# Kernel tuning notes

Hardware: AMD Instinct MI355X
Metric: run time of the kernel (lower is better)

Reference implementation:

```python
import jax, jax.numpy as jnp
import numpy as np

EPS = 0.001

def _conv1x1(h, w, b):
    # h: [n,c,v,w_dim], w: [o,c], b: [o]  -> [n,o,v,w_dim]
    return jnp.einsum('ncvw,oc->novw', h, w) + b[None, :, None, None]

def setup_inputs() -> dict:
    key = jax.random.key(0)
    ks = jax.random.split(key, 10)
    N, Cin, T, V = 16, 64, 64, 384
    inp = {
        'x': jax.random.normal(ks[0], (N, Cin, T, V), dtype=jnp.float32),
        'A': jax.random.uniform(ks[1], (N, 8, V, V), dtype=jnp.float32),
        'conv_w': jax.random.normal(ks[2], (64, Cin), dtype=jnp.float32) * 0.05,
        'conv_b': jax.random.normal(ks[3], (64,), dtype=jnp.float32) * 0.05,
        'w1': jax.random.normal(ks[4], (16, 7), dtype=jnp.float32) * 0.2,
        'b1': jax.random.normal(ks[5], (16,), dtype=jnp.float32) * 0.05,
        'w2': jax.random.normal(ks[6], (32, 16), dtype=jnp.float32) * 0.2,
        'b2': jax.random.normal(ks[7], (32,), dtype=jnp.float32) * 0.05,
        'w3': jax.random.normal(ks[8], (64, 32), dtype=jnp.float32) * 0.2,
        'b3': jax.random.normal(ks[9], (64,), dtype=jnp.float32) * 0.05,
    }
    return inp

def reference(x, A, conv_w, conv_b, w1, b1, w2, b2, w3, b3):
    # self.conv: 1x1 conv (t_kernel_size=1) mapping in_channels -> out_channels*kernel_size = 64
    x = jnp.einsum('nctv,oc->notv', x, conv_w) + conv_b[None, :, None, None]
    mask = A[:, 7][:, None]              # [n,1,v,w]
    h = A[:, :7]                         # [n,7,v,w]
    # adjmatder: three 1x1 convs with ReLU (dropout = identity in eval mode)
    h = jax.nn.relu(_conv1x1(h, w1, b1))
    h = jax.nn.relu(_conv1x1(h, w2, b2))
    h = jax.nn.relu(_conv1x1(h, w3, b3))   # [n,64,v,w]
    Am = h * mask
    Dl = 1.0 / (Am.sum(axis=2) + EPS)      # degree-inverse over v: [n,64,w]
    An = Am * Dl[:, :, None, :]            # einsum 'ncvw,ncw->ncvw'
    out = jnp.einsum('nctv,ncvw->nctw', x, An)
    return out, An
```

## Files before the change

### kernel.cpp

```cpp
#include <hip/hip_runtime.h>

#define EPS_F 0.001f

constexpr int Nn = 16;
constexpr int Cc = 64;
constexpr int Tt = 64;
constexpr int Vv = 384;
constexpr size_t TV = (size_t)Tt * Vv;
constexpr size_t VW = (size_t)Vv * Vv;
constexpr size_t OUT0 = (size_t)Nn * Cc * TV;

__global__ __launch_bounds__(256) void k_conv(const float* __restrict__ x,
        const float* __restrict__ cw, const float* __restrict__ cb,
        float* __restrict__ xc) {
    __shared__ float wt[64 * 64];
    const int tid = threadIdx.x;
    for (int i = tid; i < 4096; i += 256) {
        int o = i & 63, c = i >> 6;
        wt[c * 64 + o] = cw[o * 64 + c];
    }
    __syncthreads();
    const int b = blockIdx.x;
    const int n = b / 48;
    const int pos = (b % 48) * 512 + tid;
    const float* xin = x + (size_t)n * Cc * TV + pos;
    float acc0[64], acc1[64];
#pragma unroll
    for (int o = 0; o < 64; ++o) { acc0[o] = 0.f; acc1[o] = 0.f; }
    for (int c = 0; c < 64; ++c) {
        float x0 = xin[(size_t)c * TV];
        float x1 = xin[(size_t)c * TV + 256];
        const float4* wr = (const float4*)(wt + c * 64);
#pragma unroll
        for (int oq = 0; oq < 16; ++oq) {
            float4 w4 = wr[oq];
            acc0[oq*4+0] += x0 * w4.x; acc0[oq*4+1] += x0 * w4.y;
            acc0[oq*4+2] += x0 * w4.z; acc0[oq*4+3] += x0 * w4.w;
            acc1[oq*4+0] += x1 * w4.x; acc1[oq*4+1] += x1 * w4.y;
            acc1[oq*4+2] += x1 * w4.z; acc1[oq*4+3] += x1 * w4.w;
        }
    }
    float* xo = xc + (size_t)n * Cc * TV + pos;
#pragma unroll
    for (int o = 0; o < 64; ++o) {
        float bo = cb[o];
        xo[(size_t)o * TV]       = acc0[o] + bo;
        xo[(size_t)o * TV + 256] = acc1[o] + bo;
    }
}

__device__ __forceinline__ void mlp12(const float a[8],
        const float* __restrict__ w1, const float* __restrict__ b1,
        const float* __restrict__ w2, const float* __restrict__ b2,
        float h2[32]) {
    float h1[16];
#pragma unroll
    for (int o = 0; o < 16; ++o) {
        float t = b1[o];
#pragma unroll
        for (int k = 0; k < 7; ++k) t += w1[o * 7 + k] * a[k];
        h1[o] = fmaxf(t, 0.f);
    }
#pragma unroll
    for (int o = 0; o < 32; ++o) {
        float t = b2[o];
#pragma unroll
        for (int i = 0; i < 16; ++i) t += w2[o * 16 + i] * h1[i];
        h2[o] = fmaxf(t, 0.f);
    }
}

__global__ __launch_bounds__(384) void k_am(const float* __restrict__ A,
        const float* __restrict__ w1, const float* __restrict__ b1,
        const float* __restrict__ w2, const float* __restrict__ b2,
        const float* __restrict__ w3, const float* __restrict__ b3,
        float* __restrict__ Am) {
    const int tid = threadIdx.x;
    const int b = blockIdx.x;
    const int n = b / 384;
    const int v = b % 384;
    const float* Ab = A + (size_t)n * 8 * VW + (size_t)v * Vv + tid;
    float a[8];
#pragma unroll
    for (int k = 0; k < 8; ++k) a[k] = Ab[(size_t)k * VW];
    float h2[32];
    mlp12(a, w1, b1, w2, b2, h2);
    const float mask = a[7];
    float* ap = Am + (size_t)n * 64 * VW + (size_t)v * Vv + tid;
#pragma unroll
    for (int o = 0; o < 64; ++o) {
        float t = b3[o];
#pragma unroll
        for (int i = 0; i < 32; ++i) t += w3[o * 32 + i] * h2[i];
        ap[(size_t)o * VW] = fmaxf(t, 0.f) * mask;
    }
}

__global__ __launch_bounds__(384) void k_red(const float* __restrict__ Am,
        float* __restrict__ Dlr) {
    __shared__ float4 part[4][96];
    const int tid = threadIdx.x;
    const int wi = tid % 96;
    const int vq = tid / 96;
    const int b = blockIdx.x;
    const float4* p = (const float4*)(Am + (size_t)b * VW) + wi;
    float4 s = make_float4(0.f, 0.f, 0.f, 0.f);
#pragma unroll 4
    for (int v = vq * 96; v < vq * 96 + 96; ++v) {
        float4 t = p[(size_t)v * 96];
        s.x += t.x; s.y += t.y; s.z += t.z; s.w += t.w;
    }
    part[vq][wi] = s;
    __syncthreads();
    if (vq == 0) {
        float4 s0 = part[0][wi], s1 = part[1][wi], s2 = part[2][wi], s3 = part[3][wi];
        float4 r;
        r.x = 1.f / ((s0.x + s1.x) + (s2.x + s3.x) + EPS_F);
        r.y = 1.f / ((s0.y + s1.y) + (s2.y + s3.y) + EPS_F);
        r.z = 1.f / ((s0.z + s1.z) + (s2.z + s3.z) + EPS_F);
        r.w = 1.f / ((s0.w + s1.w) + (s2.w + s3.w) + EPS_F);
        *((float4*)(Dlr + (size_t)b * Vv) + wi) = r;
    }
}

__global__ __launch_bounds__(256) void k_gemm(const float* __restrict__ xc,
        float* __restrict__ An, const float* __restrict__ Dlr,
        float* __restrict__ out) {
    __shared__ float As[16 * 68];
    __shared__ float Bs[16 * 68];
    const int tid = threadIdx.x;
    const int b = blockIdx.x;
    const int batch = b / 6;
    const int w0 = (b % 6) * 64;
    const float* Ap = xc + (size_t)batch * TV;
    float* Bp = An + (size_t)batch * VW + w0;
    const int ty = tid / 16, tx = tid % 16;
    const int lr = tid / 4,  lq = tid % 4;
    const int br = tid / 16, bc = tid % 16;
    const float4 dl4 = *(const float4*)(Dlr + (size_t)batch * Vv + w0 + bc * 4);
    float acc[4][4];
#pragma unroll
    for (int i = 0; i < 4; ++i)
#pragma unroll
        for (int j = 0; j < 4; ++j) acc[i][j] = 0.f;
    for (int k0 = 0; k0 < 384; k0 += 16) {
        float4 a4 = *(const float4*)(Ap + (size_t)lr * 384 + k0 + lq * 4);
        float4 b4 = *(const float4*)(Bp + (size_t)(k0 + br) * 384 + bc * 4);
        b4.x *= dl4.x; b4.y *= dl4.y; b4.z *= dl4.z; b4.w *= dl4.w;
        *(float4*)(Bp + (size_t)(k0 + br) * 384 + bc * 4) = b4;
        As[(lq*4+0)*68 + lr] = a4.x;
        As[(lq*4+1)*68 + lr] = a4.y;
        As[(lq*4+2)*68 + lr] = a4.z;
        As[(lq*4+3)*68 + lr] = a4.w;
        *(float4*)(Bs + br * 68 + bc * 4) = b4;
        __syncthreads();
#pragma unroll
        for (int kk = 0; kk < 16; ++kk) {
            float4 av = *(const float4*)(As + kk * 68 + ty * 4);
            float4 bv = *(const float4*)(Bs + kk * 68 + tx * 4);
            float aa[4] = {av.x, av.y, av.z, av.w};
            float bb[4] = {bv.x, bv.y, bv.z, bv.w};
#pragma unroll
            for (int i = 0; i < 4; ++i)
#pragma unroll
                for (int j = 0; j < 4; ++j) acc[i][j] += aa[i] * bb[j];
        }
        __syncthreads();
    }
    float* op = out + (size_t)batch * TV + w0 + tx * 4;
#pragma unroll
    for (int i = 0; i < 4; ++i) {
        float4 o4 = make_float4(acc[i][0], acc[i][1], acc[i][2], acc[i][3]);
        *(float4*)(op + (size_t)(ty * 4 + i) * 384) = o4;
    }
}

extern "C" void kernel_launch(void* const* d_in, const int* in_sizes, int n_in,
                              void* d_out, int out_size, void* d_ws, size_t ws_size,
                              hipStream_t stream) {
    const float* x  = (const float*)d_in[0];
    const float* A  = (const float*)d_in[1];
    const float* cw = (const float*)d_in[2];
    const float* cb = (const float*)d_in[3];
    const float* w1 = (const float*)d_in[4];
    const float* b1 = (const float*)d_in[5];
    const float* w2 = (const float*)d_in[6];
    const float* b2 = (const float*)d_in[7];
    const float* w3 = (const float*)d_in[8];
    const float* b3 = (const float*)d_in[9];

    float* out = (float*)d_out;
    float* An  = out + OUT0;
    float* xc  = (float*)d_ws;
    float* Dlr = xc + OUT0;

    k_conv<<<768, 256, 0, stream>>>(x, cw, cb, xc);
    k_am  <<<6144, 384, 0, stream>>>(A, w1, b1, w2, b2, w3, b3, An);
    k_red <<<1024, 384, 0, stream>>>(An, Dlr);
    k_gemm<<<6144, 256, 0, stream>>>(xc, An, Dlr, out);
}
```

Baseline: 1.461 ms.

## Fuse degree reduction into GEMM and apply normalization after accumulation

Removes the separate column-sum kernel; the GEMM block accumulates column sums of Am while loading tiles, computes the inverse degree in shared memory, scales the output accumulators, then rescales An in place in a second pass. This drops one kernel launch and one global read of Am but adds a reread of the block's Am slice, which may be served from cache.

```diff
diff --git a/kernel.cpp b/kernel.cpp
--- a/kernel.cpp
+++ b/kernel.cpp
@@ -96,38 +96,12 @@
     }
 }
 
-__global__ __launch_bounds__(384) void k_red(const float* __restrict__ Am,
-        float* __restrict__ Dlr) {
-    __shared__ float4 part[4][96];
-    const int tid = threadIdx.x;
-    const int wi = tid % 96;
-    const int vq = tid / 96;
-    const int b = blockIdx.x;
-    const float4* p = (const float4*)(Am + (size_t)b * VW) + wi;
-    float4 s = make_float4(0.f, 0.f, 0.f, 0.f);
-#pragma unroll 4
-    for (int v = vq * 96; v < vq * 96 + 96; ++v) {
-        float4 t = p[(size_t)v * 96];
-        s.x += t.x; s.y += t.y; s.z += t.z; s.w += t.w;
-    }
-    part[vq][wi] = s;
-    __syncthreads();
-    if (vq == 0) {
-        float4 s0 = part[0][wi], s1 = part[1][wi], s2 = part[2][wi], s3 = part[3][wi];
-        float4 r;
-        r.x = 1.f / ((s0.x + s1.x) + (s2.x + s3.x) + EPS_F);
-        r.y = 1.f / ((s0.y + s1.y) + (s2.y + s3.y) + EPS_F);
-        r.z = 1.f / ((s0.z + s1.z) + (s2.z + s3.z) + EPS_F);
-        r.w = 1.f / ((s0.w + s1.w) + (s2.w + s3.w) + EPS_F);
-        *((float4*)(Dlr + (size_t)b * Vv) + wi) = r;
-    }
-}
-
 __global__ __launch_bounds__(256) void k_gemm(const float* __restrict__ xc,
-        float* __restrict__ An, const float* __restrict__ Dlr,
-        float* __restrict__ out) {
+        float* __restrict__ An, float* __restrict__ out) {
     __shared__ float As[16 * 68];
     __shared__ float Bs[16 * 68];
+    __shared__ float4 part[256];
+    __shared__ __align__(16) float dlr[64];
     const int tid = threadIdx.x;
     const int b = blockIdx.x;
     const int batch = b / 6;
@@ -137,17 +111,16 @@
     const int ty = tid / 16, tx = tid % 16;
     const int lr = tid / 4,  lq = tid % 4;
     const int br = tid / 16, bc = tid % 16;
-    const float4 dl4 = *(const float4*)(Dlr + (size_t)batch * Vv + w0 + bc * 4);
     float acc[4][4];
 #pragma unroll
     for (int i = 0; i < 4; ++i)
 #pragma unroll
         for (int j = 0; j < 4; ++j) acc[i][j] = 0.f;
+    float4 cs = make_float4(0.f, 0.f, 0.f, 0.f);
     for (int k0 = 0; k0 < 384; k0 += 16) {
         float4 a4 = *(const float4*)(Ap + (size_t)lr * 384 + k0 + lq * 4);
         float4 b4 = *(const float4*)(Bp + (size_t)(k0 + br) * 384 + bc * 4);
-        b4.x *= dl4.x; b4.y *= dl4.y; b4.z *= dl4.z; b4.w *= dl4.w;
-        *(float4*)(Bp + (size_t)(k0 + br) * 384 + bc * 4) = b4;
+        cs.x += b4.x; cs.y += b4.y; cs.z += b4.z; cs.w += b4.w;
         As[(lq*4+0)*68 + lr] = a4.x;
         As[(lq*4+1)*68 + lr] = a4.y;
         As[(lq*4+2)*68 + lr] = a4.z;
@@ -167,10 +140,31 @@
         }
         __syncthreads();
     }
+    part[tid] = cs;
+    __syncthreads();
+    if (tid < 64) {
+        const int q = tid >> 2, e = tid & 3;
+        float s = 0.f;
+#pragma unroll
+        for (int r = 0; r < 16; ++r) {
+            const float* p4 = (const float*)&part[r * 16 + q];
+            s += p4[e];
+        }
+        dlr[tid] = 1.f / (s + EPS_F);
+    }
+    __syncthreads();
+    const float4 d4 = *(const float4*)(dlr + tx * 4);
+    for (int k0 = 0; k0 < 384; k0 += 16) {
+        float* bp = Bp + (size_t)(k0 + br) * 384 + bc * 4;
+        float4 v = *(const float4*)bp;
+        v.x *= d4.x; v.y *= d4.y; v.z *= d4.z; v.w *= d4.w;
+        *(float4*)bp = v;
+    }
     float* op = out + (size_t)batch * TV + w0 + tx * 4;
 #pragma unroll
     for (int i = 0; i < 4; ++i) {
-        float4 o4 = make_float4(acc[i][0], acc[i][1], acc[i][2], acc[i][3]);
+        float4 o4 = make_float4(acc[i][0] * d4.x, acc[i][1] * d4.y,
+                                acc[i][2] * d4.z, acc[i][3] * d4.w);
         *(float4*)(op + (size_t)(ty * 4 + i) * 384) = o4;
     }
 }
@@ -192,10 +186,8 @@
     float* out = (float*)d_out;
     float* An  = out + OUT0;
     float* xc  = (float*)d_ws;
-    float* Dlr = xc + OUT0;
 
     k_conv<<<768, 256, 0, stream>>>(x, cw, cb, xc);
     k_am  <<<6144, 384, 0, stream>>>(A, w1, b1, w2, b2, w3, b3, An);
-    k_red <<<1024, 384, 0, stream>>>(An, Dlr);
-    k_gemm<<<6144, 256, 0, stream>>>(xc, An, Dlr, out);
+    k_gemm<<<6144, 256, 0, stream>>>(xc, An, out);
 }
```

Measured after the change: 1.431 ms. 2.0% less time.
